# Kernel optimization log

Hardware: AMD Instinct MI355X
Metric: run time of the kernel (lower is better)

Reference implementation:

```python
import jax, jax.numpy as jnp
import numpy as np

ACT_BITS = 8
W_BITS = 8
C_IN = 64


def round_ste(x):
    # straight-through rounding (Brevitas training behavior)
    return x + jax.lax.stop_gradient(jnp.round(x) - x)


def fake_quant(x, scale, bits, signed):
    if signed:
        lo, hi = -(2 ** (bits - 1)), 2 ** (bits - 1) - 1
    else:
        lo, hi = 0, 2 ** bits - 1
    return jnp.clip(round_ste(x / scale), lo, hi) * scale


def conv_nchw(x, w, pad, groups=1):
    return jax.lax.conv_general_dilated(
        x, w, window_strides=(1, 1), padding=((pad, pad), (pad, pad)),
        dimension_numbers=("NCHW", "OIHW", "NCHW"), feature_group_count=groups)


def setup_inputs() -> dict:
    key = jax.random.key(0)
    k0, k1, k2, k3 = jax.random.split(key, 4)
    x = jax.random.normal(k0, (8, 64, 112, 112), jnp.float32)
    w1 = jax.random.normal(k1, (64, 1, 3, 3), jnp.float32) * 0.05    # depthwise 3x3
    w2 = jax.random.normal(k2, (128, 64, 1, 1), jnp.float32) * 0.05  # pointwise 1x1
    w_sc = jax.random.normal(k3, (128, 64, 1, 1), jnp.float32) * 0.05  # shortcut 1x1
    sc = lambda v: jnp.asarray(v, jnp.float32)
    return dict(x=x, w1=w1, w2=w2, w_sc=w_sc,
                s_in=sc(0.03), s_relu=sc(0.02), s_add=sc(0.03),
                sw1=sc(0.004), sw2=sc(0.004), sw_sc=sc(0.004))


def reference(x, w1, w2, w_sc, s_in, s_relu, s_add, sw1, sw2, sw_sc):
    # quant_input: signed 8-bit fake-quant of the activation
    xq = fake_quant(x, s_in, ACT_BITS, True)
    # shortcut: 1x1 conv with int8 fake-quantized weights (inplane != ouplane)
    identity = conv_nchw(xq, fake_quant(w_sc, sw_sc, W_BITS, True), pad=0)
    # conv1: depthwise 3x3 (groups=inplane) with int8 fake-quantized weights
    y = conv_nchw(xq, fake_quant(w1, sw1, W_BITS, True), pad=1, groups=C_IN)
    # relu2: QuantReLU -> unsigned 8-bit fake-quant of relu
    y = fake_quant(jax.nn.relu(y), s_relu, ACT_BITS, False)
    # conv2: pointwise 1x1
    y = conv_nchw(y, fake_quant(w2, sw2, W_BITS, True), pad=0)
    # residual_add: add then requantize to signed 8-bit
    return fake_quant(y + identity, s_add, ACT_BITS, True)
```

## Files before the change

### kernel.cpp

```cpp
#include <hip/hip_runtime.h>
#include <hip/hip_bf16.h>
#include <stdint.h>

#define NIMG 8
#define CIN  64
#define HWI  12544
#define COUT 128

typedef short v8s __attribute__((ext_vector_type(8)));
typedef float v4f __attribute__((ext_vector_type(4)));

static __device__ __forceinline__ int q8(float x, float inv, float lo, float hi) {
    float t = rintf(x * inv);
    t = fminf(fmaxf(t, lo), hi);
    return (int)t;
}

static __device__ __forceinline__ uint32_t funnel(uint32_t hi, uint32_t lo, int sh) {
    return (uint32_t)(((((uint64_t)hi) << 32) | (uint64_t)lo) >> sh);
}

static __device__ __forceinline__ int dot4(uint32_t a, uint32_t b, int c) {
    int acc = c;
    #pragma unroll
    for (int i = 0; i < 4; ++i)
        acc += (int)(int8_t)(a >> (8*i)) * (int)(int8_t)(b >> (8*i));
    return acc;
}

static __device__ __forceinline__ uint16_t i2bf(int v) {
    union { float f; uint32_t u; } c; c.f = (float)v;
    return (uint16_t)(c.u >> 16);
}

__global__ void __launch_bounds__(256) wprep_kernel(
    const float* __restrict__ w2, const float* __restrict__ wsc,
    const float* __restrict__ sw2p, const float* __restrict__ swscp,
    uint16_t* __restrict__ wbuf)
{
    int t = blockIdx.x * 256 + threadIdx.x;
    int f = t * 4;
    int co = f >> 6, k = f & 63;
    float inv2 = 1.0f / sw2p[0];
    float invs = 1.0f / swscp[0];
    float4 a = *(const float4*)(w2 + f);
    float4 b = *(const float4*)(wsc + f);
    float av[4] = {a.x, a.y, a.z, a.w};
    float bv[4] = {b.x, b.y, b.z, b.w};
    uint16_t* d2 = wbuf + co*128 + k;
    uint16_t* ds = wbuf + co*128 + 64 + k;
    *(ushort2*)(d2)     = make_ushort2(i2bf(q8(av[0], inv2, -128.f, 127.f)),
                                       i2bf(q8(av[1], inv2, -128.f, 127.f)));
    *(ushort2*)(d2 + 2) = make_ushort2(i2bf(q8(av[2], inv2, -128.f, 127.f)),
                                       i2bf(q8(av[3], inv2, -128.f, 127.f)));
    *(ushort2*)(ds)     = make_ushort2(i2bf(q8(bv[0], invs, -128.f, 127.f)),
                                       i2bf(q8(bv[1], invs, -128.f, 127.f)));
    *(ushort2*)(ds + 2) = make_ushort2(i2bf(q8(bv[2], invs, -128.f, 127.f)),
                                       i2bf(q8(bv[3], invs, -128.f, 127.f)));
}

__global__ void __launch_bounds__(256, 3) fused_kernel(
    const float* __restrict__ x, const float* __restrict__ w1,
    const uint16_t* __restrict__ wbuf,
    const float* __restrict__ sinp, const float* __restrict__ srelup,
    const float* __restrict__ saddp, const float* __restrict__ sw1p,
    const float* __restrict__ sw2p, const float* __restrict__ swscp,
    float* __restrict__ out)
{
    __shared__ int8_t   tile[64 * 348];
    __shared__ uint16_t Bl[112 * 136];

    int bid = blockIdx.x;
    int n = bid / 112, h = bid - n*112;
    int tid = threadIdx.x;
    int wave = tid >> 6, lane = tid & 63;
    int lr = lane >> 4, ln = lane & 15;
    float sin_f = sinp[0];
    float inv_sin = 1.0f / sin_f;

    int c = lane;
    float isw1 = 1.0f / sw1p[0];
    uint32_t wp[3];
    #pragma unroll
    for (int ky = 0; ky < 3; ++ky) {
        uint32_t pk = 0;
        #pragma unroll
        for (int kx = 0; kx < 3; ++kx) {
            int q = q8(w1[c*9 + ky*3 + kx], isw1, -128.0f, 127.0f);
            pk |= (uint32_t)(q & 255) << (8*kx);
        }
        wp[ky] = pk;
    }

    v8s a[2][4];
    #pragma unroll
    for (int mi = 0; mi < 2; ++mi) {
        int m = (wave*2 + mi)*16 + ln;
        #pragma unroll
        for (int seg = 0; seg < 4; ++seg)
            a[mi][seg] = *(const v8s*)(wbuf + (size_t)m*128 + seg*32 + lr*8);
    }

    float4 vals[21];
    #pragma unroll
    for (int i = 0; i < 21; ++i) {
        int id = tid + i*256;
        int cc = id / 84; int rem = id - cc*84;
        int r = rem / 28; int seg = rem - r*28;
        int grow = h + r - 1;
        vals[i] = make_float4(0.f, 0.f, 0.f, 0.f);
        if ((unsigned)grow < 112u)
            vals[i] = *(const float4*)(x + ((size_t)(n*64 + cc) * HWI + grow*112 + seg*4));
    }
    #pragma unroll
    for (int i = 0; i < 21; ++i) {
        int id = tid + i*256;
        int cc = id / 84; int rem = id - cc*84;
        int r = rem / 28; int seg = rem - r*28;
        float vv[4] = {vals[i].x, vals[i].y, vals[i].z, vals[i].w};
        uint32_t pk = 0;
        #pragma unroll
        for (int e = 0; e < 4; ++e) {
            int q = q8(vv[e], inv_sin, -128.0f, 127.0f);
            pk |= (uint32_t)(q & 255) << (8*e);
        }
        *(uint32_t*)&tile[cc*348 + r*116 + seg*4] = pk;
    }
    if (tid < 192) {
        int cc = tid / 3, r = tid - cc*3;
        *(uint32_t*)&tile[cc*348 + r*116 + 112] = 0;
    }
    __syncthreads();

    {
        int w0b = wave * 28;
        float r1 = (sin_f * sw1p[0]) / srelup[0];

        int base[3];
        #pragma unroll
        for (int r2 = 0; r2 < 3; ++r2) base[r2] = c*348 + r2*116;

        uint32_t Ar[3], Br[3], Cr[3];
        #pragma unroll
        for (int r2 = 0; r2 < 3; ++r2) {
            Ar[r2] = wave ? *(uint32_t*)&tile[base[r2] + w0b - 4] : 0u;
            Br[r2] = *(uint32_t*)&tile[base[r2] + w0b];
            Cr[r2] = *(uint32_t*)&tile[base[r2] + w0b + 4];
        }

        #pragma unroll
        for (int q = 0; q < 7; ++q) {
            int acc0 = 0, acc1 = 0, acc2 = 0, acc3 = 0;
            #pragma unroll
            for (int r2 = 0; r2 < 3; ++r2) {
                uint32_t d0 = funnel(Br[r2], Ar[r2], 24);
                uint32_t d1 = Br[r2];
                uint32_t d2 = funnel(Cr[r2], Br[r2], 8);
                uint32_t d3 = funnel(Cr[r2], Br[r2], 16);
                acc0 = dot4(d0, wp[r2], acc0);
                acc1 = dot4(d1, wp[r2], acc1);
                acc2 = dot4(d2, wp[r2], acc2);
                acc3 = dot4(d3, wp[r2], acc3);
            }
            int accs[4] = {acc0, acc1, acc2, acc3};
            uint32_t xdw = Br[1];
            int pxb = w0b + q*4;
            #pragma unroll
            for (int j = 0; j < 4; ++j) {
                float t = rintf((float)accs[j] * r1);
                t = fminf(fmaxf(t, 0.0f), 255.0f);
                int xv = (int)(int8_t)((xdw >> (8*j)) & 255);
                Bl[(pxb + j)*136 + c]      = i2bf((int)t);
                Bl[(pxb + j)*136 + 64 + c] = i2bf(xv);
            }
            #pragma unroll
            for (int r2 = 0; r2 < 3; ++r2) { Ar[r2] = Br[r2]; Br[r2] = Cr[r2]; }
            if (q < 6) {
                #pragma unroll
                for (int r2 = 0; r2 < 3; ++r2)
                    Cr[r2] = *(uint32_t*)&tile[base[r2] + w0b + q*4 + 8];
            }
        }
    }
    __syncthreads();

    {
        float S2  = sw2p[0] * srelup[0];
        float Ssc = swscp[0] * sinp[0];
        float sadd = saddp[0];
        float inv_sadd = 1.0f / sadd;

        size_t orow = (size_t)n*COUT*HWI + (size_t)h*112;

        v8s bf[4];
        {
            int boff = ln*136 + lr*8;
            #pragma unroll
            for (int seg = 0; seg < 4; ++seg)
                bf[seg] = *(const v8s*)&Bl[boff + seg*32];
        }

        for (int nt = 0; nt < 7; ++nt) {
            v8s bfn[4];
            if (nt < 6) {
                int boff = ((nt+1)*16 + ln)*136 + lr*8;
                #pragma unroll
                for (int seg = 0; seg < 4; ++seg)
                    bfn[seg] = *(const v8s*)&Bl[boff + seg*32];
            }
            #pragma unroll
            for (int mi = 0; mi < 2; ++mi) {
                v4f acc2 = {0.f, 0.f, 0.f, 0.f};
                v4f accs = {0.f, 0.f, 0.f, 0.f};
                acc2 = __builtin_amdgcn_mfma_f32_16x16x32_bf16(a[mi][0], bf[0], acc2, 0, 0, 0);
                acc2 = __builtin_amdgcn_mfma_f32_16x16x32_bf16(a[mi][1], bf[1], acc2, 0, 0, 0);
                accs = __builtin_amdgcn_mfma_f32_16x16x32_bf16(a[mi][2], bf[2], accs, 0, 0, 0);
                accs = __builtin_amdgcn_mfma_f32_16x16x32_bf16(a[mi][3], bf[3], accs, 0, 0, 0);
                size_t obase = orow + (size_t)((wave*2 + mi)*16 + lr*4)*HWI + nt*16 + ln;
                #pragma unroll
                for (int r = 0; r < 4; ++r) {
                    float v = S2 * acc2[r] + Ssc * accs[r];
                    float t = rintf(v * inv_sadd);
                    t = fminf(fmaxf(t, -128.0f), 127.0f);
                    out[obase + (size_t)r*HWI] = t * sadd;
                }
            }
            if (nt < 6) {
                #pragma unroll
                for (int seg = 0; seg < 4; ++seg) bf[seg] = bfn[seg];
            }
        }
    }
}

extern "C" void kernel_launch(void* const* d_in, const int* in_sizes, int n_in,
                              void* d_out, int out_size, void* d_ws, size_t ws_size,
                              hipStream_t stream) {
    const float* x     = (const float*)d_in[0];
    const float* w1    = (const float*)d_in[1];
    const float* w2    = (const float*)d_in[2];
    const float* wsc   = (const float*)d_in[3];
    const float* sin   = (const float*)d_in[4];
    const float* srelu = (const float*)d_in[5];
    const float* sadd  = (const float*)d_in[6];
    const float* sw1   = (const float*)d_in[7];
    const float* sw2   = (const float*)d_in[8];
    const float* swsc  = (const float*)d_in[9];

    uint16_t* wbuf = (uint16_t*)d_ws;

    wprep_kernel<<<8, 256, 0, stream>>>(w2, wsc, sw2, swsc, wbuf);
    fused_kernel<<<NIMG * 112, 256, 0, stream>>>(x, w1, wbuf,
                                                 sin, srelu, sadd, sw1, sw2, swsc,
                                                 (float*)d_out);
}
```

Baseline: 128.8 us.

## Store intermediate tile as int8 in LDS and raise occupancy to four blocks

```diff
diff --git a/kernel.cpp b/kernel.cpp
--- a/kernel.cpp
+++ b/kernel.cpp
@@ -59,7 +59,7 @@
                                        i2bf(q8(bv[3], invs, -128.f, 127.f)));
 }
 
-__global__ void __launch_bounds__(256, 3) fused_kernel(
+__global__ void __launch_bounds__(256, 4) fused_kernel(
     const float* __restrict__ x, const float* __restrict__ w1,
     const uint16_t* __restrict__ wbuf,
     const float* __restrict__ sinp, const float* __restrict__ srelup,
@@ -67,8 +67,8 @@
     const float* __restrict__ sw2p, const float* __restrict__ swscp,
     float* __restrict__ out)
 {
-    __shared__ int8_t   tile[64 * 348];
-    __shared__ uint16_t Bl[112 * 136];
+    __shared__ int8_t tile[64 * 348];
+    __shared__ int8_t Bl[112 * 132];
 
     int bid = blockIdx.x;
     int n = bid / 112, h = bid - n*112;
@@ -101,30 +101,33 @@
             a[mi][seg] = *(const v8s*)(wbuf + (size_t)m*128 + seg*32 + lr*8);
     }
 
-    float4 vals[21];
-    #pragma unroll
-    for (int i = 0; i < 21; ++i) {
-        int id = tid + i*256;
-        int cc = id / 84; int rem = id - cc*84;
-        int r = rem / 28; int seg = rem - r*28;
-        int grow = h + r - 1;
-        vals[i] = make_float4(0.f, 0.f, 0.f, 0.f);
-        if ((unsigned)grow < 112u)
-            vals[i] = *(const float4*)(x + ((size_t)(n*64 + cc) * HWI + grow*112 + seg*4));
-    }
-    #pragma unroll
-    for (int i = 0; i < 21; ++i) {
-        int id = tid + i*256;
-        int cc = id / 84; int rem = id - cc*84;
-        int r = rem / 28; int seg = rem - r*28;
-        float vv[4] = {vals[i].x, vals[i].y, vals[i].z, vals[i].w};
-        uint32_t pk = 0;
-        #pragma unroll
-        for (int e = 0; e < 4; ++e) {
-            int q = q8(vv[e], inv_sin, -128.0f, 127.0f);
-            pk |= (uint32_t)(q & 255) << (8*e);
-        }
-        *(uint32_t*)&tile[cc*348 + r*116 + seg*4] = pk;
+    #pragma unroll
+    for (int b = 0; b < 3; ++b) {
+        float4 vals[7];
+        #pragma unroll
+        for (int i = 0; i < 7; ++i) {
+            int id = tid + (b*7 + i)*256;
+            int cc = id / 84; int rem = id - cc*84;
+            int r = rem / 28; int seg = rem - r*28;
+            int grow = h + r - 1;
+            vals[i] = make_float4(0.f, 0.f, 0.f, 0.f);
+            if ((unsigned)grow < 112u)
+                vals[i] = *(const float4*)(x + ((size_t)(n*64 + cc) * HWI + grow*112 + seg*4));
+        }
+        #pragma unroll
+        for (int i = 0; i < 7; ++i) {
+            int id = tid + (b*7 + i)*256;
+            int cc = id / 84; int rem = id - cc*84;
+            int r = rem / 28; int seg = rem - r*28;
+            float vv[4] = {vals[i].x, vals[i].y, vals[i].z, vals[i].w};
+            uint32_t pk = 0;
+            #pragma unroll
+            for (int e = 0; e < 4; ++e) {
+                int q = q8(vv[e], inv_sin, -128.0f, 127.0f);
+                pk |= (uint32_t)(q & 255) << (8*e);
+            }
+            *(uint32_t*)&tile[cc*348 + r*116 + seg*4] = pk;
+        }
     }
     if (tid < 192) {
         int cc = tid / 3, r = tid - cc*3;
@@ -169,9 +172,8 @@
             for (int j = 0; j < 4; ++j) {
                 float t = rintf((float)accs[j] * r1);
                 t = fminf(fmaxf(t, 0.0f), 255.0f);
-                int xv = (int)(int8_t)((xdw >> (8*j)) & 255);
-                Bl[(pxb + j)*136 + c]      = i2bf((int)t);
-                Bl[(pxb + j)*136 + 64 + c] = i2bf(xv);
+                Bl[(pxb + j)*132 + c]      = (int8_t)(int)t;
+                Bl[(pxb + j)*132 + 64 + c] = (int8_t)((xdw >> (8*j)) & 255);
             }
             #pragma unroll
             for (int r2 = 0; r2 < 3; ++r2) { Ar[r2] = Br[r2]; Br[r2] = Cr[r2]; }
@@ -192,21 +194,28 @@
 
         size_t orow = (size_t)n*COUT*HWI + (size_t)h*112;
 
-        v8s bf[4];
-        {
-            int boff = ln*136 + lr*8;
-            #pragma unroll
-            for (int seg = 0; seg < 4; ++seg)
-                bf[seg] = *(const v8s*)&Bl[boff + seg*32];
-        }
-
         for (int nt = 0; nt < 7; ++nt) {
-            v8s bfn[4];
-            if (nt < 6) {
-                int boff = ((nt+1)*16 + ln)*136 + lr*8;
-                #pragma unroll
-                for (int seg = 0; seg < 4; ++seg)
-                    bfn[seg] = *(const v8s*)&Bl[boff + seg*32];
+            int boff = (nt*16 + ln)*132 + lr*8;
+            v8s bf[4];
+            #pragma unroll
+            for (int seg = 0; seg < 4; ++seg) {
+                uint32_t d0 = *(const uint32_t*)&Bl[boff + seg*32];
+                uint32_t d1 = *(const uint32_t*)&Bl[boff + seg*32 + 4];
+                v8s t;
+                if (seg < 2) {
+                    #pragma unroll
+                    for (int e = 0; e < 4; ++e) {
+                        t[e]     = (short)i2bf((int)((d0 >> (8*e)) & 255u));
+                        t[4 + e] = (short)i2bf((int)((d1 >> (8*e)) & 255u));
+                    }
+                } else {
+                    #pragma unroll
+                    for (int e = 0; e < 4; ++e) {
+                        t[e]     = (short)i2bf((int)(int8_t)(d0 >> (8*e)));
+                        t[4 + e] = (short)i2bf((int)(int8_t)(d1 >> (8*e)));
+                    }
+                }
+                bf[seg] = t;
             }
             #pragma unroll
             for (int mi = 0; mi < 2; ++mi) {
@@ -225,10 +234,6 @@
                     out[obase + (size_t)r*HWI] = t * sadd;
                 }
             }
-            if (nt < 6) {
-                #pragma unroll
-                for (int seg = 0; seg < 4; ++seg) bf[seg] = bfn[seg];
-            }
         }
     }
 }
```

Result: faster. 118.7 us (-7.8%).
